# Optimization experiments

Hardware: AMD Instinct MI355X
Metric: run time of the kernel (lower is better)

The kernel has to match this reference:

```python
import jax, jax.numpy as jnp
import numpy as np

B, D = 65536, 1024
E = 10   # experts per group (shared and per-task)
H = 10   # expert hidden units
T = 2    # tasks
G = 20   # gate units = task experts + shared experts


def setup_inputs() -> dict:
    key = jax.random.key(0)
    ks = jax.random.split(key, 8)
    s = 1.0 / np.sqrt(D)
    return {
        "x": jax.random.normal(ks[0], (B, D), dtype=jnp.float32),
        "show_index": jax.random.randint(ks[1], (B,), 0, 100, dtype=jnp.int64),
        "st": jax.random.normal(ks[2], (B, 8), dtype=jnp.float32),
        "Ws": jax.random.normal(ks[3], (E, D, H), dtype=jnp.float32) * s,
        "bs": jnp.zeros((E, H), dtype=jnp.float32),
        "Wt": jax.random.normal(ks[4], (T, E, D, H), dtype=jnp.float32) * s,
        "bt": jnp.zeros((T, E, H), dtype=jnp.float32),
        "Wg": jax.random.normal(ks[5], (T, D, G), dtype=jnp.float32) * s,
        "bg": jnp.zeros((T, G), dtype=jnp.float32),
        "Wc": jax.random.normal(ks[6], (H, 1), dtype=jnp.float32),
        "bc": jnp.zeros((1,), dtype=jnp.float32),
        "Wv": jax.random.normal(ks[7], (H, 1), dtype=jnp.float32),
        "bv": jnp.zeros((1,), dtype=jnp.float32),
    }


def reference(x, show_index, st, Ws, bs, Wt, bt, Wg, bg, Wc, bc, Wv, bv):
    # shared experts: [B, H, E]  (Dense(H,relu) per expert, stacked on axis 2)
    share = jax.nn.relu(jnp.einsum('bd,edh->bhe', x, Ws) + bs.T)

    def task_tower(i):
        gate = jax.nn.softmax(x @ Wg[i] + bg[i], axis=-1)               # [B, G]
        task = jax.nn.relu(jnp.einsum('bd,edh->bhe', x, Wt[i]) + bt[i].T)  # [B, H, E]
        merge = jnp.concatenate([task, share], axis=2)                  # [B, H, G]
        # gate broadcast over H (repeat_elements on axis 1), sum over experts
        return jnp.sum(merge * gate[:, None, :], axis=2)                # [B, H]

    f0 = task_tower(0)
    f1 = task_tower(1)
    ctr_logits = jax.nn.sigmoid(f0 @ Wc + bc)  # [B, 1]
    cvr_logits = jax.nn.sigmoid(f1 @ Wv + bv)  # [B, 1]
    return (ctr_logits, cvr_logits)
```

## Files before the change

kernel.cpp:

```cpp
#include <hip/hip_runtime.h>
#include <hip/hip_bf16.h>

typedef __attribute__((ext_vector_type(8))) short bf16x8;
typedef __attribute__((ext_vector_type(4))) float f32x4;

#define NCOLP 384
#define STEP_SHORTS (NCOLP * 32)
#define STEP_BYTES 24576
#define SEG_BYTES 6144
#define NSTEP 32
#define HSTEP 16
#define BROWS 65536

static __device__ __forceinline__ unsigned int bf16rne(float f) {
  unsigned int u = __float_as_uint(f);
  return (u + 0x7FFFu + ((u >> 16) & 1u)) >> 16;
}
static __device__ __forceinline__ unsigned int pack2(float a, float b) {
  return bf16rne(a) | (bf16rne(b) << 16);
}

__global__ void ple_prep(const float* __restrict__ Ws, const float* __restrict__ bs,
                         const float* __restrict__ Wt, const float* __restrict__ bt,
                         const float* __restrict__ Wg, const float* __restrict__ bg,
                         unsigned short* __restrict__ Wpack, float* __restrict__ bias) {
  const int n = blockIdx.x;
  const int tid = threadIdx.x;
  const float* src = nullptr;
  int stride = 0;
  float bval = 0.f;
  if (n < 200) {
    int t = n / 100, m = n % 100, e = m / 10, h = m % 10;
    src = Wt + (size_t)(t * 10 + e) * 10240 + h;
    stride = 10;
    bval = bt[(t * 10 + e) * 10 + h];
  } else if (n < 300) {
    int m = n - 200, e = m / 10, h = m % 10;
    src = Ws + (size_t)e * 10240 + h;
    stride = 10;
    bval = bs[e * 10 + h];
  } else if (n < 340) {
    int m = n - 300, t = m / 20, g = m % 20;
    src = Wg + (size_t)t * 20480 + g;
    stride = 20;
    bval = bg[t * 20 + g];
  }
  for (int j = 0; j < 4; j++) {
    int k = tid + j * 256;
    float v = src ? src[(size_t)k * stride] : 0.f;
    Wpack[(size_t)(k >> 5) * STEP_SHORTS + ((k >> 3) & 3) * (NCOLP * 8) + n * 8 +
          (k & 7)] = (unsigned short)bf16rne(v);
  }
  if (tid == 0 && n < 352) bias[n] = bval;
}

__global__ __launch_bounds__(256, 2) void ple_main(
    const float* __restrict__ x, const unsigned short* __restrict__ Wpack,
    const float* __restrict__ bias, const float* __restrict__ Wc,
    const float* __restrict__ bc, const float* __restrict__ Wv,
    const float* __restrict__ bv, float* __restrict__ out) {
  __shared__ __align__(16) char smem[65536];
  float* z = (float*)smem;

  const int tid = threadIdx.x;
  const int l = tid & 63, w = tid >> 6;
  const int arow = l & 15, ablk = l >> 4;
  const int rowbase = blockIdx.x * 64;
  const int h0 = (int)(blockIdx.x & 1);

  const f32x4 fzero = {0.f, 0.f, 0.f, 0.f};
  f32x4 acc[4][6];
#pragma unroll
  for (int i = 0; i < 4; ++i)
#pragma unroll
    for (int j = 0; j < 6; ++j) acc[i][j] = fzero;

  const char* bbase = (const char*)Wpack + ablk * SEG_BYTES +
                      (w * 96 + arow) * 16;
  bf16x8 b0[6], b1[6], b2[6];

#pragma unroll
  for (int nt = 0; nt < 6; nt++) {
    b0[nt] = *(const bf16x8*)(bbase + (size_t)(((h0 << 4) + 0) & 31) *
                                          STEP_BYTES + nt * 256);
    b1[nt] = *(const bf16x8*)(bbase + (size_t)(((h0 << 4) + 1) & 31) *
                                          STEP_BYTES + nt * 256);
  }

#define STEPX(I, BU, BP)                                                       \
  {                                                                            \
    const int ipre = ((I) + 2 <= 31) ? (I) + 2 : 31;                           \
    const int kpre = ((h0 << 4) + ipre) & 31;                                  \
    const char* bp = bbase + (size_t)kpre * STEP_BYTES;                        \
    _Pragma("unroll") for (int nt = 0; nt < 6; nt++)                           \
        BP[nt] = *(const bf16x8*)(bp + nt * 256);                              \
    _Pragma("unroll") for (int mf = 0; mf < 4; mf++) {                         \
      const int ksl = (I)&15;                                                  \
      const bf16x8 av = *(const bf16x8*)(smem + (mf * 16 + arow) * 1024 +      \
                                         (((ksl * 4 + ablk) ^ (arow & 7)) *    \
                                          16));                                \
      _Pragma("unroll") for (int nt = 0; nt < 6; nt++)                         \
          acc[mf][nt] = __builtin_amdgcn_mfma_f32_16x16x32_bf16(               \
              av, BU[nt], acc[mf][nt], 0, 0, 0);                               \
    }                                                                          \
  }

#define SLOAD(J, FA, FB)                                                       \
  const float4 FA = *(const float4*)(xb + (size_t)(J) * 4 * 4096);             \
  const float4 FB = *(const float4*)(xb + (size_t)(J) * 4 * 4096 + 16);
#define SWRITE(J, FA, FB)                                                      \
  {                                                                            \
    const int row = w + (J)*4;                                                 \
    char* dst = smem + row * 1024 + ((l ^ (row & 7)) * 16);                    \
    *(uint4*)dst = make_uint4(pack2(FA.x, FA.y), pack2(FA.z, FA.w),            \
                              pack2(FB.x, FB.y), pack2(FB.z, FB.w));           \
  }

#pragma unroll
  for (int hh = 0; hh < 2; ++hh) {
    const int half = h0 ^ hh;
    {
      const char* xb = (const char*)x + (size_t)(rowbase + w) * 4096 +
                       (size_t)half * 2048 + l * 32;
      {
        SLOAD(0, a0, c0) SLOAD(1, a1, c1) SLOAD(2, a2, c2)
        SLOAD(3, a3, c3) SLOAD(4, a4, c4) SLOAD(5, a5, c5)
        SWRITE(0, a0, c0) SWRITE(1, a1, c1) SWRITE(2, a2, c2)
        SWRITE(3, a3, c3) SWRITE(4, a4, c4) SWRITE(5, a5, c5)
      }
      {
        SLOAD(6, a0, c0) SLOAD(7, a1, c1) SLOAD(8, a2, c2)
        SLOAD(9, a3, c3) SLOAD(10, a4, c4) SLOAD(11, a5, c5)
        SWRITE(6, a0, c0) SWRITE(7, a1, c1) SWRITE(8, a2, c2)
        SWRITE(9, a3, c3) SWRITE(10, a4, c4) SWRITE(11, a5, c5)
      }
      {
        SLOAD(12, a0, c0) SLOAD(13, a1, c1) SLOAD(14, a2, c2)
        SLOAD(15, a3, c3)
        SWRITE(12, a0, c0) SWRITE(13, a1, c1) SWRITE(14, a2, c2)
        SWRITE(15, a3, c3)
      }
    }
    __syncthreads();

    if (hh == 0) {
      STEPX(0, b0, b2)  STEPX(1, b1, b0)  STEPX(2, b2, b1)
      STEPX(3, b0, b2)  STEPX(4, b1, b0)  STEPX(5, b2, b1)
      STEPX(6, b0, b2)  STEPX(7, b1, b0)  STEPX(8, b2, b1)
      STEPX(9, b0, b2)  STEPX(10, b1, b0) STEPX(11, b2, b1)
      STEPX(12, b0, b2) STEPX(13, b1, b0) STEPX(14, b2, b1)
      STEPX(15, b0, b2)
    } else {
      STEPX(16, b1, b0) STEPX(17, b2, b1) STEPX(18, b0, b2)
      STEPX(19, b1, b0) STEPX(20, b2, b1) STEPX(21, b0, b2)
      STEPX(22, b1, b0) STEPX(23, b2, b1) STEPX(24, b0, b2)
      STEPX(25, b1, b0) STEPX(26, b2, b1) STEPX(27, b0, b2)
      STEPX(28, b1, b0) STEPX(29, b2, b1) STEPX(30, b0, b2)
      STEPX(31, b1, b0)
    }
    __syncthreads();
  }
#undef STEPX
#undef SLOAD
#undef SWRITE

#pragma unroll
  for (int p = 0; p < 2; p++) {
    __syncthreads();
#pragma unroll
    for (int q = 0; q < 2; q++) {
      const int mf = p * 2 + q;
#pragma unroll
      for (int nt = 0; nt < 6; nt++) {
        if (w == 3 && nt >= 4) continue;
#pragma unroll
        for (int r = 0; r < 4; r++)
          z[(q * 16 + ablk * 4 + r) * 357 + w * 96 + nt * 16 + arow] =
              acc[mf][nt][r];
      }
    }
    __syncthreads();
    {
      const int item = tid >> 2, sub = tid & 3;
      const int t = item >> 5, r = item & 31;
      const float* zr = &z[r * 357];
      float gl[5], m = -1e30f;
#pragma unroll
      for (int v = 0; v < 5; v++) {
        const int u = sub * 5 + v;
        gl[v] = zr[300 + t * 20 + u] + bias[300 + t * 20 + u];
        m = fmaxf(m, gl[v]);
      }
      m = fmaxf(m, __shfl_xor(m, 1));
      m = fmaxf(m, __shfl_xor(m, 2));
      const float* Wl = t ? Wv : Wc;
      float wl[10];
#pragma unroll
      for (int h = 0; h < 10; h++) wl[h] = Wl[h];
      float s = 0.f, accum = 0.f;
#pragma unroll
      for (int v = 0; v < 5; v++) {
        const int u = sub * 5 + v;
        const float pu = __expf(gl[v] - m);
        s += pu;
        const int cbase = (u < 10) ? (t * 100 + u * 10) : (200 + (u - 10) * 10);
        float d = 0.f;
#pragma unroll
        for (int h = 0; h < 10; h++)
          d += fmaxf(zr[cbase + h] + bias[cbase + h], 0.f) * wl[h];
        accum += pu * d;
      }
      s += __shfl_xor(s, 1);
      s += __shfl_xor(s, 2);
      accum += __shfl_xor(accum, 1);
      accum += __shfl_xor(accum, 2);
      if (sub == 0) {
        const float logit = (t ? bv[0] : bc[0]) + accum / s;
        out[(size_t)t * BROWS + rowbase + p * 32 + r] =
            1.f / (1.f + __expf(-logit));
      }
    }
  }
}

extern "C" void kernel_launch(void* const* d_in, const int* in_sizes, int n_in,
                              void* d_out, int out_size, void* d_ws, size_t ws_size,
                              hipStream_t stream) {
  const float* x = (const float*)d_in[0];
  const float* Ws = (const float*)d_in[3];
  const float* bs = (const float*)d_in[4];
  const float* Wt = (const float*)d_in[5];
  const float* bt = (const float*)d_in[6];
  const float* Wg = (const float*)d_in[7];
  const float* bg = (const float*)d_in[8];
  const float* Wc = (const float*)d_in[9];
  const float* bc = (const float*)d_in[10];
  const float* Wv = (const float*)d_in[11];
  const float* bv = (const float*)d_in[12];
  unsigned short* Wpack = (unsigned short*)d_ws;
  float* bias = (float*)((char*)d_ws + (size_t)NCOLP * 1024 * 2);
  float* out = (float*)d_out;

  hipLaunchKernelGGL(ple_prep, dim3(NCOLP), dim3(256), 0, stream, Ws, bs, Wt, bt,
                     Wg, bg, Wpack, bias);
  hipLaunchKernelGGL(ple_main, dim3(BROWS / 64), dim3(256), 0, stream, x, Wpack,
                     bias, Wc, bc, Wv, bv, out);
}
```

Measured before the change: 81.30 us.

## Double-buffer x quarters in LDS and overlap global loads with MFMA steps

Splits the K dimension into four quarters staged in two ping-pong LDS buffers. Global loads and bf16 writes for the next quarter are interleaved with MFMA steps on the current one, using sched_barrier and lightweight barriers. This drops the per-block half-order alternation and the bulk load-then-compute phases, aiming to hide x load latency behind compute. The trade-off is more register pressure from in-flight float4 staging and a fragile hand-written schedule with manual waitcnt.

Result: no change. 79.76 us (-1.9%).

```diff
diff --git a/kernel.cpp b/kernel.cpp
--- a/kernel.cpp
+++ b/kernel.cpp
@@ -9,8 +9,8 @@
 #define STEP_BYTES 24576
 #define SEG_BYTES 6144
 #define NSTEP 32
-#define HSTEP 16
 #define BROWS 65536
+#define QSZ 32768
 
 static __device__ __forceinline__ unsigned int bf16rne(float f) {
   unsigned int u = __float_as_uint(f);
@@ -59,14 +59,13 @@
     const float* __restrict__ bias, const float* __restrict__ Wc,
     const float* __restrict__ bc, const float* __restrict__ Wv,
     const float* __restrict__ bv, float* __restrict__ out) {
-  __shared__ __align__(16) char smem[65536];
+  __shared__ __align__(16) char smem[2 * QSZ];
   float* z = (float*)smem;
 
   const int tid = threadIdx.x;
   const int l = tid & 63, w = tid >> 6;
   const int arow = l & 15, ablk = l >> 4;
   const int rowbase = blockIdx.x * 64;
-  const int h0 = (int)(blockIdx.x & 1);
 
   const f32x4 fzero = {0.f, 0.f, 0.f, 0.f};
   f32x4 acc[4][6];
@@ -81,88 +80,87 @@
 
 #pragma unroll
   for (int nt = 0; nt < 6; nt++) {
-    b0[nt] = *(const bf16x8*)(bbase + (size_t)(((h0 << 4) + 0) & 31) *
-                                          STEP_BYTES + nt * 256);
-    b1[nt] = *(const bf16x8*)(bbase + (size_t)(((h0 << 4) + 1) & 31) *
-                                          STEP_BYTES + nt * 256);
-  }
-
+    b0[nt] = *(const bf16x8*)(bbase + nt * 256);
+    b1[nt] = *(const bf16x8*)(bbase + STEP_BYTES + nt * 256);
+  }
+
+  const char* xstage = (const char*)x + (size_t)(rowbase + w) * 4096 + l * 16;
+  float4 g[8], hgrp[8];
+
+#define GISSUE(Q, G, J0)                                                       \
+  {                                                                            \
+    _Pragma("unroll") for (int j = 0; j < 8; j++)                              \
+        G[j] = *(const float4*)(xstage + (size_t)((J0) + j) * 4 * 4096 +       \
+                                (Q)*1024);                                     \
+  }
+#define GWRITE(Q, G, J0)                                                       \
+  {                                                                            \
+    _Pragma("unroll") for (int j = 0; j < 8; j++) {                            \
+      const int row = w + ((J0) + j) * 4;                                      \
+      const int s = l >> 1;                                                    \
+      const int segp = (s & 24) | ((s & 7) ^ (row & 7));                       \
+      uint2 u;                                                                 \
+      u.x = pack2(G[j].x, G[j].y);                                             \
+      u.y = pack2(G[j].z, G[j].w);                                             \
+      *(uint2*)(smem + ((Q)&1) * QSZ + row * 512 + segp * 16 + (l & 1) * 8) =  \
+          u;                                                                   \
+    }                                                                          \
+  }
 #define STEPX(I, BU, BP)                                                       \
   {                                                                            \
     const int ipre = ((I) + 2 <= 31) ? (I) + 2 : 31;                           \
-    const int kpre = ((h0 << 4) + ipre) & 31;                                  \
-    const char* bp = bbase + (size_t)kpre * STEP_BYTES;                        \
+    const char* bp = bbase + (size_t)ipre * STEP_BYTES;                        \
     _Pragma("unroll") for (int nt = 0; nt < 6; nt++)                           \
         BP[nt] = *(const bf16x8*)(bp + nt * 256);                              \
     _Pragma("unroll") for (int mf = 0; mf < 4; mf++) {                         \
-      const int ksl = (I)&15;                                                  \
-      const bf16x8 av = *(const bf16x8*)(smem + (mf * 16 + arow) * 1024 +      \
-                                         (((ksl * 4 + ablk) ^ (arow & 7)) *    \
-                                          16));                                \
+      const int s = ((I)&7) * 4 + ablk;                                        \
+      const int segp = (s & 24) | ((s & 7) ^ (arow & 7));                      \
+      const bf16x8 av =                                                        \
+          *(const bf16x8*)(smem + (((I) >> 3) & 1) * QSZ +                     \
+                           (mf * 16 + arow) * 512 + segp * 16);                \
       _Pragma("unroll") for (int nt = 0; nt < 6; nt++)                         \
           acc[mf][nt] = __builtin_amdgcn_mfma_f32_16x16x32_bf16(               \
               av, BU[nt], acc[mf][nt], 0, 0, 0);                               \
     }                                                                          \
   }
-
-#define SLOAD(J, FA, FB)                                                       \
-  const float4 FA = *(const float4*)(xb + (size_t)(J) * 4 * 4096);             \
-  const float4 FB = *(const float4*)(xb + (size_t)(J) * 4 * 4096 + 16);
-#define SWRITE(J, FA, FB)                                                      \
-  {                                                                            \
-    const int row = w + (J)*4;                                                 \
-    char* dst = smem + row * 1024 + ((l ^ (row & 7)) * 16);                    \
-    *(uint4*)dst = make_uint4(pack2(FA.x, FA.y), pack2(FA.z, FA.w),            \
-                              pack2(FB.x, FB.y), pack2(FB.z, FB.w));           \
-  }
-
-#pragma unroll
-  for (int hh = 0; hh < 2; ++hh) {
-    const int half = h0 ^ hh;
-    {
-      const char* xb = (const char*)x + (size_t)(rowbase + w) * 4096 +
-                       (size_t)half * 2048 + l * 32;
-      {
-        SLOAD(0, a0, c0) SLOAD(1, a1, c1) SLOAD(2, a2, c2)
-        SLOAD(3, a3, c3) SLOAD(4, a4, c4) SLOAD(5, a5, c5)
-        SWRITE(0, a0, c0) SWRITE(1, a1, c1) SWRITE(2, a2, c2)
-        SWRITE(3, a3, c3) SWRITE(4, a4, c4) SWRITE(5, a5, c5)
-      }
-      {
-        SLOAD(6, a0, c0) SLOAD(7, a1, c1) SLOAD(8, a2, c2)
-        SLOAD(9, a3, c3) SLOAD(10, a4, c4) SLOAD(11, a5, c5)
-        SWRITE(6, a0, c0) SWRITE(7, a1, c1) SWRITE(8, a2, c2)
-        SWRITE(9, a3, c3) SWRITE(10, a4, c4) SWRITE(11, a5, c5)
-      }
-      {
-        SLOAD(12, a0, c0) SLOAD(13, a1, c1) SLOAD(14, a2, c2)
-        SLOAD(15, a3, c3)
-        SWRITE(12, a0, c0) SWRITE(13, a1, c1) SWRITE(14, a2, c2)
-        SWRITE(15, a3, c3)
-      }
-    }
-    __syncthreads();
-
-    if (hh == 0) {
-      STEPX(0, b0, b2)  STEPX(1, b1, b0)  STEPX(2, b2, b1)
-      STEPX(3, b0, b2)  STEPX(4, b1, b0)  STEPX(5, b2, b1)
-      STEPX(6, b0, b2)  STEPX(7, b1, b0)  STEPX(8, b2, b1)
-      STEPX(9, b0, b2)  STEPX(10, b1, b0) STEPX(11, b2, b1)
-      STEPX(12, b0, b2) STEPX(13, b1, b0) STEPX(14, b2, b1)
-      STEPX(15, b0, b2)
-    } else {
-      STEPX(16, b1, b0) STEPX(17, b2, b1) STEPX(18, b0, b2)
-      STEPX(19, b1, b0) STEPX(20, b2, b1) STEPX(21, b0, b2)
-      STEPX(22, b1, b0) STEPX(23, b2, b1) STEPX(24, b0, b2)
-      STEPX(25, b1, b0) STEPX(26, b2, b1) STEPX(27, b0, b2)
-      STEPX(28, b1, b0) STEPX(29, b2, b1) STEPX(30, b0, b2)
-      STEPX(31, b1, b0)
-    }
-    __syncthreads();
-  }
+#define SB __builtin_amdgcn_sched_barrier(0);
+#define QBAR                                                                   \
+  asm volatile("s_waitcnt lgkmcnt(0)" ::: "memory");                           \
+  __builtin_amdgcn_s_barrier();
+
+  GISSUE(0, g, 0) SB GWRITE(0, g, 0) SB GISSUE(0, hgrp, 8) SB
+  GWRITE(0, hgrp, 8) QBAR SB
+
+  STEPX(0, b0, b2) STEPX(1, b1, b0)
+  SB GISSUE(1, g, 0) SB
+  STEPX(2, b2, b1) STEPX(3, b0, b2) STEPX(4, b1, b0)
+  SB GWRITE(1, g, 0) SB GISSUE(1, hgrp, 8) SB
+  STEPX(5, b2, b1) STEPX(6, b0, b2) STEPX(7, b1, b0)
+  SB GWRITE(1, hgrp, 8) QBAR SB
+
+  STEPX(8, b2, b1) STEPX(9, b0, b2)
+  SB GISSUE(2, g, 0) SB
+  STEPX(10, b1, b0) STEPX(11, b2, b1) STEPX(12, b0, b2)
+  SB GWRITE(2, g, 0) SB GISSUE(2, hgrp, 8) SB
+  STEPX(13, b1, b0) STEPX(14, b2, b1) STEPX(15, b0, b2)
+  SB GWRITE(2, hgrp, 8) QBAR SB
+
+  STEPX(16, b1, b0) STEPX(17, b2, b1)
+  SB GISSUE(3, g, 0) SB
+  STEPX(18, b0, b2) STEPX(19, b1, b0) STEPX(20, b2, b1)
+  SB GWRITE(3, g, 0) SB GISSUE(3, hgrp, 8) SB
+  STEPX(21, b0, b2) STEPX(22, b1, b0) STEPX(23, b2, b1)
+  SB GWRITE(3, hgrp, 8) QBAR SB
+
+  STEPX(24, b0, b2) STEPX(25, b1, b0) STEPX(26, b2, b1) STEPX(27, b0, b2)
+  STEPX(28, b1, b0) STEPX(29, b2, b1) STEPX(30, b0, b2) STEPX(31, b1, b0)
+  QBAR
+
+#undef QBAR
+#undef SB
 #undef STEPX
-#undef SLOAD
-#undef SWRITE
+#undef GWRITE
+#undef GISSUE
 
 #pragma unroll
   for (int p = 0; p < 2; p++) {
```
